# Kernel tuning notes

Hardware: AMD Instinct MI355X
Metric: run time of the kernel (lower is better)

Reference implementation:

```python
import jax, jax.numpy as jnp
import numpy as np


def gcn_conv(x, src, dst, W, b, n_nodes):
    # PyG GCNConv with self-loops and symmetric normalization.
    h = x @ W                                        # [N, out]
    deg = jax.ops.segment_sum(jnp.ones_like(dst, dtype=h.dtype), dst,
                              num_segments=n_nodes)  # includes self-loops
    dinv = jnp.where(deg > 0, jax.lax.rsqrt(deg), 0.0)
    norm = dinv[src] * dinv[dst]                     # [E]
    msg = h[src] * norm[:, None]                     # gather + scale
    out = jax.ops.segment_sum(msg, dst, num_segments=n_nodes)
    return out + b


def setup_inputs() -> dict:
    key = jax.random.key(0)
    ks = jax.random.split(key, 16)
    N, E, F_IN, H, H2, C = 150000, 2400000, 61, 32, 16, 3
    x = jax.random.normal(ks[0], (N, F_IN), dtype=jnp.float32)
    edge_index = jax.random.randint(ks[1], (2, E), 0, N, dtype=jnp.int64)

    def lin(k, fin, fout):
        kw, kb = jax.random.split(k)
        s = 1.0 / np.sqrt(fin)
        W = jax.random.uniform(kw, (fin, fout), jnp.float32, -s, s)
        b = jax.random.uniform(kb, (fout,), jnp.float32, -s, s)
        return W, b

    W1, b1 = lin(ks[2], F_IN, H)
    W2, b2 = lin(ks[3], H, H)
    W3, b3 = lin(ks[4], H, H)
    W4, b4 = lin(ks[5], H, H)
    Wl1, bl1 = lin(ks[6], H, H2)
    Wl2, bl2 = lin(ks[7], H2, C)
    return {"x": x, "edge_index": edge_index,
            "W1": W1, "b1": b1, "W2": W2, "b2": b2,
            "W3": W3, "b3": b3, "W4": W4, "b4": b4,
            "Wl1": Wl1, "bl1": bl1, "Wl2": Wl2, "bl2": bl2}


def reference(x, edge_index, W1, b1, W2, b2, W3, b3, W4, b4, Wl1, bl1, Wl2, bl2):
    n = x.shape[0]
    loops = jnp.arange(n, dtype=edge_index.dtype)
    src = jnp.concatenate([edge_index[0], loops])
    dst = jnp.concatenate([edge_index[1], loops])
    # dropout p=0.25 is identity in eval mode
    h = jax.nn.relu(gcn_conv(x, src, dst, W1, b1, n))
    h = jax.nn.relu(gcn_conv(h, src, dst, W2, b2, n))
    h = jax.nn.relu(gcn_conv(h, src, dst, W3, b3, n))
    h = jax.nn.relu(gcn_conv(h, src, dst, W4, b4, n))
    g = jnp.sum(h, axis=0)                           # sum pool over all nodes -> [32]
    g = jax.nn.relu(g @ Wl1 + bl1)
    return g @ Wl2 + bl2                             # [3]
```

## Files before the change

### kernel.cpp

```cpp
#include <hip/hip_runtime.h>
#include <hip/hip_fp16.h>

#define F_IN 61
#define H 32
#define BUCK_BITS 8
#define BUCK_SZ   256
#define CHUNK     8192
#define XPAD 72
#define CMAX 6144

typedef _Float16 f16x8 __attribute__((ext_vector_type(8)));
typedef float    f32x4 __attribute__((ext_vector_type(4)));

__global__ __launch_bounds__(256) void scan1_kernel(const int* __restrict__ in,
                                                    int* __restrict__ scanned,
                                                    int* __restrict__ btot, int n) {
    __shared__ int s[256];
    int tid = threadIdx.x;
    int i = blockIdx.x * 256 + tid;
    int v = (i < n) ? in[i] : 0;
    s[tid] = v;
    __syncthreads();
    for (int off = 1; off < 256; off <<= 1) {
        int t = (tid >= off) ? s[tid - off] : 0;
        __syncthreads();
        s[tid] += t;
        __syncthreads();
    }
    if (i < n) scanned[i] = s[tid] - v;
    if (tid == 255) btot[blockIdx.x] = s[255];
}

__global__ __launch_bounds__(1024) void scan2_kernel(int* __restrict__ btot, int nB) {
    __shared__ int s[1024];
    int tid = threadIdx.x;
    int v = (tid < nB) ? btot[tid] : 0;
    s[tid] = v;
    __syncthreads();
    for (int off = 1; off < 1024; off <<= 1) {
        int t = (tid >= off) ? s[tid - off] : 0;
        __syncthreads();
        s[tid] += t;
        __syncthreads();
    }
    if (tid < nB) btot[tid] = s[tid] - v;
}

__global__ __launch_bounds__(256) void histA_kernel(const int* __restrict__ ei,
                                                    int* __restrict__ counts,
                                                    float* __restrict__ gs,
                                                    int E, int B, int nbuck) {
    __shared__ int h[640];
    int tid = threadIdx.x;
    if (blockIdx.x == 0) {
        #pragma unroll
        for (int r = 0; r < 8; r++) gs[r * 256 + tid] = 0.f;
    }
    for (int i = tid; i < nbuck; i += 256) h[i] = 0;
    __syncthreads();
    int e0 = blockIdx.x * CHUNK;
    int e1 = e0 + CHUNK; if (e1 > E) e1 = E;
    for (int e = e0 + tid; e < e1; e += 256)
        atomicAdd(&h[ei[E + e] >> BUCK_BITS], 1);
    __syncthreads();
    for (int i = tid; i < nbuck; i += 256) counts[i * B + blockIdx.x] = h[i];
}

__global__ __launch_bounds__(256) void binB_kernel(const int* __restrict__ ei,
                                                   const int* __restrict__ countsS,
                                                   const int* __restrict__ btot,
                                                   int* __restrict__ tmp,
                                                   int E, int B, int nbuck) {
    __shared__ int lcur[640];
    int tid = threadIdx.x;
    for (int i = tid; i < nbuck; i += 256) {
        int ci = i * B + blockIdx.x;
        lcur[i] = countsS[ci] + btot[ci >> 8];
    }
    __syncthreads();
    int e0 = blockIdx.x * CHUNK;
    int e1 = e0 + CHUNK; if (e1 > E) e1 = E;
    for (int e = e0 + tid; e < e1; e += 256) {
        int s = ei[e];
        int d = ei[E + e];
        int pos = atomicAdd(&lcur[d >> BUCK_BITS], 1);
        tmp[pos] = (s << BUCK_BITS) | (d & (BUCK_SZ - 1));
    }
}

__global__ __launch_bounds__(256) void binC_kernel(const int* __restrict__ countsS,
                                                   const int* __restrict__ btot,
                                                   const int* __restrict__ tmp,
                                                   int* __restrict__ src_sorted,
                                                   int* __restrict__ row_start,
                                                   float* __restrict__ dinv,
                                                   __half* __restrict__ bufA,
                                                   __half* __restrict__ bufB,
                                                   int N, int E, int B, int nbuck) {
    __shared__ int hist[BUCK_SZ];
    __shared__ int pre[BUCK_SZ];
    __shared__ int lcur[BUCK_SZ];
    __shared__ int ebuf[CMAX];
    __shared__ int obuf[CMAX];
    int tid = threadIdx.x;
    int b = blockIdx.x;
    int base = b << BUCK_BITS;
    if (b == 0 && tid < H) {
        bufA[(size_t)N * H + tid] = __float2half(0.f);
        bufB[(size_t)N * H + tid] = __float2half(0.f);
    }
    int c0 = b * B;
    int e0 = countsS[c0] + btot[c0 >> 8];
    int e1 = E;
    if (b + 1 < nbuck) {
        int c1 = (b + 1) * B;
        e1 = countsS[c1] + btot[c1 >> 8];
    }
    int cnt = e1 - e0;
    bool fits = (cnt <= CMAX);
    hist[tid] = 0;
    __syncthreads();
    if (fits) {
        for (int j = tid; j < cnt; j += 256) {
            int p = tmp[e0 + j];
            ebuf[j] = p;
            atomicAdd(&hist[p & (BUCK_SZ - 1)], 1);
        }
    } else {
        for (int j = tid; j < cnt; j += 256)
            atomicAdd(&hist[tmp[e0 + j] & (BUCK_SZ - 1)], 1);
    }
    __syncthreads();
    int v = hist[tid];
    pre[tid] = v;
    __syncthreads();
    for (int off = 1; off < 256; off <<= 1) {
        int t = (tid >= off) ? pre[tid - off] : 0;
        __syncthreads();
        pre[tid] += t;
        __syncthreads();
    }
    int excl = pre[tid] - v;
    int node = base + tid;
    if (node < N) {
        row_start[node] = e0 + excl;
        dinv[node] = rsqrtf((float)v + 1.0f);
        if (node == N - 1) row_start[N] = E;
    }
    lcur[tid] = fits ? excl : (e0 + excl);
    __syncthreads();
    if (fits) {
        for (int j = tid; j < cnt; j += 256) {
            int p = ebuf[j];
            int pos = atomicAdd(&lcur[p & (BUCK_SZ - 1)], 1);
            obuf[pos] = (p >> BUCK_BITS) << 6;
        }
        __syncthreads();
        for (int j = tid; j < cnt; j += 256)
            src_sorted[e0 + j] = obuf[j];
    } else {
        for (int j = tid; j < cnt; j += 256) {
            int p = tmp[e0 + j];
            int pos = atomicAdd(&lcur[p & (BUCK_SZ - 1)], 1);
            src_sorted[pos] = (p >> BUCK_BITS) << 6;
        }
    }
}

__global__ __launch_bounds__(256) void gemm1_kernel(const float* __restrict__ x,
                                                    const float* __restrict__ W,
                                                    const float* __restrict__ dinv,
                                                    __half* __restrict__ h, int N) {
    __shared__ _Float16 Wt[H * XPAD];
    __shared__ _Float16 xs[64 * XPAD];
    int tid = threadIdx.x;
    for (int i = tid; i < 2048; i += 256) {
        int k = i >> 5, f = i & 31;
        Wt[f * XPAD + k] = (k < F_IN) ? (_Float16)W[k * H + f] : (_Float16)0.f;
    }
    int nb = blockIdx.x * 64;
    int navail = N - nb; if (navail > 64) navail = 64;
    int lim = navail * F_IN;
    const float* xb = x + (long long)nb * F_IN;
    for (int i = tid; i < 64 * F_IN; i += 256) {
        int n = i / F_IN, k = i - n * F_IN;
        xs[n * XPAD + k] = (i < lim) ? (_Float16)xb[i] : (_Float16)0.f;
    }
    if (tid < 192) {
        int n = tid / 3, k = F_IN + (tid - n * 3);
        xs[n * XPAD + k] = (_Float16)0.f;
    }
    __syncthreads();
    int w = tid >> 6, lane = tid & 63;
    int l16 = lane & 15, g = lane >> 4;
    const f16x8* ax  = (const f16x8*)&xs[(w * 16 + l16) * XPAD + g * 8];
    const f16x8* bw0 = (const f16x8*)&Wt[l16 * XPAD + g * 8];
    const f16x8* bw1 = (const f16x8*)&Wt[(16 + l16) * XPAD + g * 8];
    f16x8 a0 = ax[0],  a1 = ax[4];
    f16x8 b00 = bw0[0], b01 = bw0[4];
    f16x8 b10 = bw1[0], b11 = bw1[4];
    f32x4 acc0 = {0.f, 0.f, 0.f, 0.f};
    f32x4 acc1 = {0.f, 0.f, 0.f, 0.f};
    acc0 = __builtin_amdgcn_mfma_f32_16x16x32_f16(a0, b00, acc0, 0, 0, 0);
    acc0 = __builtin_amdgcn_mfma_f32_16x16x32_f16(a1, b01, acc0, 0, 0, 0);
    acc1 = __builtin_amdgcn_mfma_f32_16x16x32_f16(a0, b10, acc1, 0, 0, 0);
    acc1 = __builtin_amdgcn_mfma_f32_16x16x32_f16(a1, b11, acc1, 0, 0, 0);
    int nodebase = nb + w * 16 + g * 4;
    #pragma unroll
    for (int r = 0; r < 4; r++) {
        int node = nodebase + r;
        if (node < N) {
            float di = dinv[node];
            h[(long long)node * H + l16]      = __float2half(acc0[r] * di);
            h[(long long)node * H + 16 + l16] = __float2half(acc1[r] * di);
        }
    }
}

__global__ __launch_bounds__(256) void agg_gemm_kernel(const int* __restrict__ row_start,
                                                       const int* __restrict__ src_sorted,
                                                       const float* __restrict__ dinv,
                                                       const __half* __restrict__ hs,
                                                       const float* __restrict__ b,
                                                       const float* __restrict__ Wn,
                                                       __half* __restrict__ hout, int N) {
    __shared__ float Ws[H * H];
    __shared__ float t[8 * H];
    int tid = threadIdx.x;
    for (int i = tid; i < H * H; i += 256) Ws[i] = Wn[i];
    int nl = tid >> 5;
    int lane32 = tid & 31;
    int p = lane32 >> 4;
    int fp = lane32 & 15;
    int node = blockIdx.x * 8 + nl;
    int zoff = N << 6;
    __half2 accA = __floats2half2_rn(0.f, 0.f);
    __half2 accB = __floats2half2_rn(0.f, 0.f);
    if (node < N) {
        const char* hbase = (const char*)hs + (fp << 2);
        int e0 = row_start[node], e1 = row_start[node + 1];
        int idxv = (e0 + lane32 < e1) ? src_sorted[e0 + lane32] : zoff;
        for (int base = e0; base < e1; base += 32) {
            int w = e1 - base; if (w > 32) w = 32;
            int idxN = (base + 32 + lane32 < e1) ? src_sorted[base + 32 + lane32] : zoff;
            for (int j = 0; j < w; j += 16) {
                int offs[8];
                #pragma unroll
                for (int k = 0; k < 8; k++) offs[k] = __shfl(idxv, j + 2 * k + p, 32);
                unsigned g[8];
                #pragma unroll
                for (int k = 0; k < 8; k++) g[k] = *(const unsigned*)(hbase + offs[k]);
                #pragma unroll
                for (int k = 0; k < 8; k += 2) {
                    accA = __hadd2(accA, *(__half2*)&g[k]);
                    accB = __hadd2(accB, *(__half2*)&g[k + 1]);
                }
            }
            idxv = idxN;
        }
    }
    __half2 accH = __hadd2(accA, accB);
    float2 acc = __half22float2(accH);
    acc.x += __shfl_xor(acc.x, 16, 32);
    acc.y += __shfl_xor(acc.y, 16, 32);
    if (node < N && p == 0) {
        float di = dinv[node];
        unsigned sv = *(const unsigned*)((const char*)hs + ((long long)node << 6) + (fp << 2));
        float2 s2 = __half22float2(*(__half2*)&sv);
        float2 bv = ((const float2*)b)[fp];
        float rx = fmaxf(di * (acc.x + s2.x) + bv.x, 0.f);
        float ry = fmaxf(di * (acc.y + s2.y) + bv.y, 0.f);
        ((float2*)&t[nl * H])[fp] = make_float2(rx, ry);
    }
    __syncthreads();
    if (node < N) {
        int f = lane32;
        float s = 0.f;
        #pragma unroll
        for (int k = 0; k < H; k++) s += t[nl * H + k] * Ws[k * H + f];
        hout[(long long)node * H + f] = __float2half(s * dinv[node]);
    }
}

__global__ __launch_bounds__(256) void agg_pool_kernel(const int* __restrict__ row_start,
                                                       const int* __restrict__ src_sorted,
                                                       const float* __restrict__ dinv,
                                                       const __half* __restrict__ hs,
                                                       const float* __restrict__ b,
                                                       float* __restrict__ gs, int N) {
    __shared__ float t[8 * H];
    int tid = threadIdx.x;
    int nl = tid >> 5;
    int lane32 = tid & 31;
    int p = lane32 >> 4;
    int fp = lane32 & 15;
    int node = blockIdx.x * 8 + nl;
    int zoff = N << 6;
    __half2 accA = __floats2half2_rn(0.f, 0.f);
    __half2 accB = __floats2half2_rn(0.f, 0.f);
    if (node < N) {
        const char* hbase = (const char*)hs + (fp << 2);
        int e0 = row_start[node], e1 = row_start[node + 1];
        int idxv = (e0 + lane32 < e1) ? src_sorted[e0 + lane32] : zoff;
        for (int base = e0; base < e1; base += 32) {
            int w = e1 - base; if (w > 32) w = 32;
            int idxN = (base + 32 + lane32 < e1) ? src_sorted[base + 32 + lane32] : zoff;
            for (int j = 0; j < w; j += 16) {
                int offs[8];
                #pragma unroll
                for (int k = 0; k < 8; k++) offs[k] = __shfl(idxv, j + 2 * k + p, 32);
                unsigned g[8];
                #pragma unroll
                for (int k = 0; k < 8; k++) g[k] = *(const unsigned*)(hbase + offs[k]);
                #pragma unroll
                for (int k = 0; k < 8; k += 2) {
                    accA = __hadd2(accA, *(__half2*)&g[k]);
                    accB = __hadd2(accB, *(__half2*)&g[k + 1]);
                }
            }
            idxv = idxN;
        }
    }
    __half2 accH = __hadd2(accA, accB);
    float2 acc = __half22float2(accH);
    acc.x += __shfl_xor(acc.x, 16, 32);
    acc.y += __shfl_xor(acc.y, 16, 32);
    if (p == 0) {
        float2 r = make_float2(0.f, 0.f);
        if (node < N) {
            float di = dinv[node];
            unsigned sv = *(const unsigned*)((const char*)hs + ((long long)node << 6) + (fp << 2));
            float2 s2 = __half22float2(*(__half2*)&sv);
            float2 bv = ((const float2*)b)[fp];
            r.x = fmaxf(di * (acc.x + s2.x) + bv.x, 0.f);
            r.y = fmaxf(di * (acc.y + s2.y) + bv.y, 0.f);
        }
        ((float2*)&t[nl * H])[fp] = r;
    }
    __syncthreads();
    if (tid < H) {
        float s = 0.f;
        #pragma unroll
        for (int rI = 0; rI < 8; rI++) s += t[rI * H + tid];
        atomicAdd(&gs[(blockIdx.x & 63) * H + tid], s);
    }
}

__global__ __launch_bounds__(64) void head_kernel(const float* __restrict__ gs,
                                                  const float* __restrict__ Wl1,
                                                  const float* __restrict__ bl1,
                                                  const float* __restrict__ Wl2,
                                                  const float* __restrict__ bl2,
                                                  float* __restrict__ out) {
    __shared__ float gg[H];
    __shared__ float t[16];
    int tid = threadIdx.x;
    if (tid < H) {
        float s = 0.f;
        for (int c = 0; c < 64; c++) s += gs[c * H + tid];
        gg[tid] = s;
    }
    __syncthreads();
    if (tid < 16) {
        float s = bl1[tid];
        #pragma unroll
        for (int k = 0; k < 32; k++) s += gg[k] * Wl1[k * 16 + tid];
        t[tid] = fmaxf(s, 0.f);
    }
    __syncthreads();
    if (tid < 3) {
        float s = bl2[tid];
        #pragma unroll
        for (int k = 0; k < 16; k++) s += t[k] * Wl2[k * 3 + tid];
        out[tid] = s;
    }
}

extern "C" void kernel_launch(void* const* d_in, const int* in_sizes, int n_in,
                              void* d_out, int out_size, void* d_ws, size_t ws_size,
                              hipStream_t stream) {
    const float* x   = (const float*)d_in[0];
    const int*   ei  = (const int*)d_in[1];
    const float* W1  = (const float*)d_in[2];
    const float* b1  = (const float*)d_in[3];
    const float* W2  = (const float*)d_in[4];
    const float* b2  = (const float*)d_in[5];
    const float* W3  = (const float*)d_in[6];
    const float* b3  = (const float*)d_in[7];
    const float* W4  = (const float*)d_in[8];
    const float* b4  = (const float*)d_in[9];
    const float* Wl1 = (const float*)d_in[10];
    const float* bl1 = (const float*)d_in[11];
    const float* Wl2 = (const float*)d_in[12];
    const float* bl2 = (const float*)d_in[13];
    float* out = (float*)d_out;

    const int N = in_sizes[0] / F_IN;
    const int E = in_sizes[1] / 2;
    const int nbuck = (N + BUCK_SZ - 1) >> BUCK_BITS;
    const int B = (E + CHUNK - 1) / CHUNK;
    const int nC = nbuck * B;

    char* ws = (char*)d_ws;
    size_t off = 0;
    auto alloc = [&](size_t bytes) {
        char* p = ws + off;
        off += (bytes + 255) & ~(size_t)255;
        return p;
    };
    float* dinv       = (float*)alloc((size_t)N * 4);
    int*   row_start  = (int*)alloc((size_t)(N + 1) * 4);
    int*   counts     = (int*)alloc((size_t)nC * 4);
    int*   countsS    = (int*)alloc((size_t)nC * 4);
    int*   btot2      = (int*)alloc(((size_t)nC / 256 + 2) * 4);
    int*   src_sorted = (int*)alloc((size_t)E * 4);
    int*   tmp        = (int*)alloc((size_t)E * 4);
    __half* bufA      = (__half*)alloc((size_t)(N + 1) * H * 2);
    __half* bufB      = (__half*)alloc((size_t)(N + 1) * H * 2);
    float* gs         = (float*)alloc(64 * H * 4);

    const int TB = 256;
    const int gC  = (nC + TB - 1) / TB;
    const int gN8 = (N + 7) / 8;
    const int gN64 = (N + 63) / 64;

    histA_kernel<<<B, TB, 0, stream>>>(ei, counts, gs, E, B, nbuck);
    scan1_kernel<<<gC, TB, 0, stream>>>(counts, countsS, btot2, nC);
    scan2_kernel<<<1, 1024, 0, stream>>>(btot2, gC);
    binB_kernel<<<B, TB, 0, stream>>>(ei, countsS, btot2, tmp, E, B, nbuck);
    binC_kernel<<<nbuck, TB, 0, stream>>>(countsS, btot2, tmp, src_sorted, row_start,
                                          dinv, bufA, bufB, N, E, B, nbuck);

    gemm1_kernel<<<gN64, TB, 0, stream>>>(x, W1, dinv, bufA, N);
    agg_gemm_kernel<<<gN8, TB, 0, stream>>>(row_start, src_sorted, dinv, bufA, b1, W2, bufB, N);
    agg_gemm_kernel<<<gN8, TB, 0, stream>>>(row_start, src_sorted, dinv, bufB, b2, W3, bufA, N);
    agg_gemm_kernel<<<gN8, TB, 0, stream>>>(row_start, src_sorted, dinv, bufA, b3, W4, bufB, N);
    agg_pool_kernel<<<gN8, TB, 0, stream>>>(row_start, src_sorted, dinv, bufB, b4, gs, N);

    head_kernel<<<1, 64, 0, stream>>>(gs, Wl1, bl1, Wl2, bl2, out);
}
```

Baseline: 355.8 us.

## Stage bucket scatter in shared memory for coalesced global writes

The bucketing pass now first builds a local histogram and exclusive scan of each chunk's edges by bucket in LDS. It then scatters the packed edges into an LDS buffer ordered by bucket and writes them to global memory in order, using a per-bucket offset. Consecutive threads therefore write mostly contiguous addresses, replacing the random global scatter. The cost is a second histogram pass over the destination indices, extra LDS use (about 50KB), and several block-wide barriers for the scan.

After: 353.5 us. Within noise of the previous version (-0.7%).

```diff
diff --git a/kernel.cpp b/kernel.cpp
--- a/kernel.cpp
+++ b/kernel.cpp
@@ -71,21 +71,55 @@
                                                    const int* __restrict__ btot,
                                                    int* __restrict__ tmp,
                                                    int E, int B, int nbuck) {
+    __shared__ int gshift[640];
+    __shared__ int lhist[640];
     __shared__ int lcur[640];
-    int tid = threadIdx.x;
-    for (int i = tid; i < nbuck; i += 256) {
-        int ci = i * B + blockIdx.x;
-        lcur[i] = countsS[ci] + btot[ci >> 8];
-    }
-    __syncthreads();
+    __shared__ int ebuf[CHUNK];
+    __shared__ unsigned short bbuf[CHUNK];
+    __shared__ int sc[256];
+    int tid = threadIdx.x;
+    for (int i = tid; i < 640; i += 256) lhist[i] = 0;
     int e0 = blockIdx.x * CHUNK;
     int e1 = e0 + CHUNK; if (e1 > E) e1 = E;
+    int cnt = e1 - e0;
+    __syncthreads();
+    for (int e = e0 + tid; e < e1; e += 256)
+        atomicAdd(&lhist[ei[E + e] >> BUCK_BITS], 1);
+    __syncthreads();
+    int carry = 0;
+    for (int s0 = 0; s0 < 640; s0 += 256) {
+        int idx = s0 + tid;
+        int v = (idx < 640) ? lhist[idx] : 0;
+        sc[tid] = v;
+        __syncthreads();
+        for (int off = 1; off < 256; off <<= 1) {
+            int t = (tid >= off) ? sc[tid - off] : 0;
+            __syncthreads();
+            sc[tid] += t;
+            __syncthreads();
+        }
+        int excl = sc[tid] - v + carry;
+        if (idx < 640) {
+            lcur[idx] = excl;
+            if (idx < nbuck) {
+                int ci = idx * B + blockIdx.x;
+                gshift[idx] = (countsS[ci] + btot[ci >> 8]) - excl;
+            }
+        }
+        carry += sc[255];
+        __syncthreads();
+    }
     for (int e = e0 + tid; e < e1; e += 256) {
         int s = ei[e];
         int d = ei[E + e];
-        int pos = atomicAdd(&lcur[d >> BUCK_BITS], 1);
-        tmp[pos] = (s << BUCK_BITS) | (d & (BUCK_SZ - 1));
-    }
+        int b = d >> BUCK_BITS;
+        int lp = atomicAdd(&lcur[b], 1);
+        ebuf[lp] = (s << BUCK_BITS) | (d & (BUCK_SZ - 1));
+        bbuf[lp] = (unsigned short)b;
+    }
+    __syncthreads();
+    for (int j = tid; j < cnt; j += 256)
+        tmp[j + gshift[bbuf[j]]] = ebuf[j];
 }
 
 __global__ __launch_bounds__(256) void binC_kernel(const int* __restrict__ countsS,
```
